# Optimization experiments

Measured on AMD Instinct MI355X. Metric: run time of the kernel, lower is better.

## Reference

```python
import jax, jax.numpy as jnp
import numpy as np
from jax import lax

B, C_IN, C_OUT, KK, KS = 8, 32, 64, 4, 3
D, H, W = 32, 64, 64
PAD = 1

def setup_inputs() -> dict:
    key = jax.random.key(0)
    ks = jax.random.split(key, 12)
    s = 0.02
    return {
        "x": jax.random.normal(ks[0], (B, C_IN, D, H, W), jnp.float32),
        # K candidate conv kernels and biases
        "weight": jax.random.normal(ks[1], (KK, C_OUT, C_IN, KS, KS, KS), jnp.float32) * s,
        "cbias": jnp.zeros((KK, C_OUT), jnp.float32),
        "temperature": jnp.float32(34.0),
        # attention key path: BN(affine, eval-mode) -> GELU -> 1x1 conv (linear)
        "bn1_g": jnp.ones((C_IN,), jnp.float32),
        "bn1_b": jnp.zeros((C_IN,), jnp.float32),
        "w1": jax.random.normal(ks[2], (C_IN, C_IN), jnp.float32) * s,
        "b1": jnp.zeros((C_IN,), jnp.float32),
        "bn2_g": jnp.ones((C_IN,), jnp.float32),
        "bn2_b": jnp.zeros((C_IN,), jnp.float32),
        "w2": jax.random.normal(ks[3], (C_IN, C_IN), jnp.float32) * s,
        "b2": jnp.zeros((C_IN,), jnp.float32),
        "bn3_g": jnp.ones((C_IN,), jnp.float32),
        "bn3_b": jnp.zeros((C_IN,), jnp.float32),
        "w3": jax.random.normal(ks[4], (KK, C_IN), jnp.float32) * s,
        "b3": jnp.zeros((KK,), jnp.float32),
    }

def _attention(p, temperature, bn1_g, bn1_b, w1, b1, bn2_g, bn2_b, w2, b2, bn3_g, bn3_b, w3, b3):
    # p: [B, C] pooled features. 1x1x1 convs on 1x1x1 maps == linear layers.
    gelu = lambda t: jax.nn.gelu(t, approximate=False)  # torch nn.GELU default is erf
    a = gelu(p * bn1_g + bn1_b)          # BN (eval: rm=0, rv=1) + GELU
    a = a @ w1.T + b1
    a = gelu(a * bn2_g + bn2_b)
    a = a @ w2.T + b2
    a = a + p                            # ResidualLayer (plain add)
    a = a * bn3_g + bn3_b
    logits = a @ w3.T + b3               # [B, K]
    return jax.nn.softmax(logits / temperature, axis=1)

def reference(x, weight, cbias, temperature, bn1_g, bn1_b, w1, b1,
              bn2_g, bn2_b, w2, b2, bn3_g, bn3_b, w3, b3):
    # x: [B, C_in, D, H, W]
    p = x.mean(axis=(2, 3, 4))  # AdaptiveAvgPool3d(1)
    attn = _attention(p, temperature, bn1_g, bn1_b, w1, b1,
                      bn2_g, bn2_b, w2, b2, bn3_g, bn3_b, w3, b3)  # [B, K]
    # per-sample aggregated kernels / bias
    agg_w = jnp.einsum('bk,koidhw->boidhw', attn, weight)  # [B, O, I, k, k, k]
    agg_b = attn @ cbias                                    # [B, O]
    # grouped-conv trick (groups=B) == per-sample conv3d -> vmap over batch
    def conv1(xi, wi):
        return lax.conv_general_dilated(
            xi[None], wi, window_strides=(1, 1, 1),
            padding=[(PAD, PAD)] * 3,
            dimension_numbers=('NCDHW', 'OIDHW', 'NCDHW'))[0]
    out = jax.vmap(conv1)(x, agg_w)  # [B, O, D, H, W]
    return out + agg_b[:, :, None, None, None]
```

## Files before the change

kernel.cpp:

```cpp
#include <hip/hip_runtime.h>
#include <hip/hip_bf16.h>
#include <math.h>

#define B_   8
#define CIN  32
#define COUT 64
#define KK_  4
#define DD   32
#define HH   64
#define WW   64
#define HW   (HH*WW)
#define DHW  (DD*HH*WW)

typedef __attribute__((ext_vector_type(8)))  short bf16x8;
typedef __attribute__((ext_vector_type(16))) float f32x16;

__device__ __forceinline__ unsigned short f2bf(float f) {
    union { float f; unsigned int u; } v; v.f = f;
    return (unsigned short)((v.u + 0x7FFFu + ((v.u >> 16) & 1u)) >> 16);
}
__device__ __forceinline__ void gll16(const void* g, void* l) {
    __builtin_amdgcn_global_load_lds(
        (const __attribute__((address_space(1))) void*)g,
        (__attribute__((address_space(3))) void*)l, 16, 0, 0);
}

__global__ __launch_bounds__(256) void transpose_kernel(const float* __restrict__ x,
                                                        unsigned short* __restrict__ xt,
                                                        float* __restrict__ pblk) {
    const int t = threadIdx.x;
    const int r = t >> 6, w = t & 63;
    const int hb = blockIdx.x;
    const int h = (hb << 2) + r;
    const int d = blockIdx.y, b = blockIdx.z;

    const float* xb = x + (size_t)b*CIN*DHW + (size_t)d*HW + (size_t)h*WW + w;
    float f[CIN];
    #pragma unroll
    for (int c = 0; c < CIN; ++c) f[c] = xb[(size_t)c * DHW];

    unsigned int packed[CIN/2];
    #pragma unroll
    for (int c2 = 0; c2 < CIN/2; ++c2) {
        unsigned int lo = f2bf(f[2*c2]);
        unsigned int hi = f2bf(f[2*c2+1]);
        packed[c2] = lo | (hi << 16);
    }
    char* row = (char*)xt + (size_t)((b*DD + d)*HH + h) * 4096;
    #pragma unroll
    for (int q = 0; q < 4; ++q) {
        uint4 v = make_uint4(packed[4*q], packed[4*q+1], packed[4*q+2], packed[4*q+3]);
        *(uint4*)(row + q*1024 + (((w << 4)) ^ (q << 4))) = v;
    }

    #pragma unroll
    for (int off = 32; off > 0; off >>= 1) {
        #pragma unroll
        for (int c = 0; c < CIN; ++c) f[c] += __shfl_xor(f[c], off);
    }
    __shared__ float ws4[4][CIN];
    if ((t & 63) < CIN) ws4[r][t & 63] = f[t & 63];
    __syncthreads();
    if (t < CIN)
        pblk[(size_t)((b*DD + d)*16 + hb)*CIN + t] =
            ws4[0][t] + ws4[1][t] + ws4[2][t] + ws4[3][t];
}

__device__ __forceinline__ float gelu_erf(float v) {
    return 0.5f * v * (1.f + erff(v * 0.70710678118654752f));
}

__global__ void attn_kernel(const float* __restrict__ pblk,
                            const float* __restrict__ temperature,
                            const float* __restrict__ bn1_g, const float* __restrict__ bn1_b,
                            const float* __restrict__ w1,    const float* __restrict__ b1,
                            const float* __restrict__ bn2_g, const float* __restrict__ bn2_b,
                            const float* __restrict__ w2,    const float* __restrict__ b2,
                            const float* __restrict__ bn3_g, const float* __restrict__ bn3_b,
                            const float* __restrict__ w3,    const float* __restrict__ b3,
                            const float* __restrict__ cbias,
                            float* __restrict__ attn_out, float* __restrict__ aggb_out) {
    __shared__ float A[B_][CIN], A2[B_][CIN];
    __shared__ float L[B_][KK_], ATT[B_][KK_];
    const int t = threadIdx.x;
    const int b = t >> 5, c = t & 31;

    float pv = 0.f;
    for (int i = 0; i < DD*16; ++i) pv += pblk[(size_t)(b*DD*16 + i)*CIN + c];
    pv *= (1.f / (float)DHW);

    A[b][c] = gelu_erf(pv * bn1_g[c] + bn1_b[c]);
    __syncthreads();

    float s = b1[c];
    for (int j = 0; j < CIN; ++j) s += A[b][j] * w1[c*CIN + j];
    A2[b][c] = gelu_erf(s * bn2_g[c] + bn2_b[c]);
    __syncthreads();

    float s2 = b2[c];
    for (int j = 0; j < CIN; ++j) s2 += A2[b][j] * w2[c*CIN + j];
    s2 += pv;
    s2 = s2 * bn3_g[c] + bn3_b[c];
    __syncthreads();
    A[b][c] = s2;
    __syncthreads();

    if (c < KK_) {
        float lv = b3[c];
        for (int j = 0; j < CIN; ++j) lv += A[b][j] * w3[c*CIN + j];
        L[b][c] = lv;
    }
    __syncthreads();

    const float T = temperature[0];
    if (c < KK_) {
        float m = fmaxf(fmaxf(L[b][0], L[b][1]), fmaxf(L[b][2], L[b][3]));
        float e = expf((L[b][c] - m) / T);
        float den = 0.f;
        for (int j = 0; j < KK_; ++j) den += expf((L[b][j] - m) / T);
        float av = e / den;
        ATT[b][c] = av;
        attn_out[b*KK_ + c] = av;
    }
    __syncthreads();

    for (int o = c; o < COUT; o += CIN) {
        float sb = 0.f;
        for (int k = 0; k < KK_; ++k) sb += ATT[b][k] * cbias[k*COUT + o];
        aggb_out[b*COUT + o] = sb;
    }
}

__global__ void aggw_kernel(const float* __restrict__ weight,
                            const float* __restrict__ attn,
                            unsigned short* __restrict__ wt) {
    const int idx = blockIdx.x * 256 + threadIdx.x;
    const int ci   = idx & 31;
    const int co   = (idx >> 5) & 63;
    int r          = idx >> 11;
    const int kpos = r % 27;
    const int b    = r / 27;
    float s = 0.f;
    #pragma unroll
    for (int k = 0; k < KK_; ++k)
        s += attn[b*KK_ + k] * weight[((k*COUT + co)*CIN + ci)*27 + kpos];
    wt[idx] = f2bf(s);
}

__global__ __launch_bounds__(128, 1) void conv_mfma(const unsigned short* __restrict__ xt,
                                                    const unsigned short* __restrict__ wt,
                                                    const float* __restrict__ aggb,
                                                    float* __restrict__ out) {
    __shared__ char smem[19 * 4096];
    const int t    = threadIdx.x;
    const int lane = t & 63;
    const int wv   = t >> 6;
    const int lw   = lane & 31, lh = lane >> 5;

    const int id = blockIdx.x;
    const int b  = id & 7;
    const int h  = (id >> 3) & 63;
    const int d0 = ((id >> 9) & 7) << 2;

    const char* xb  = (const char*)xt + (size_t)(b*DD)*HH*4096;
    const char* wtb = (const char*)wt + (size_t)b * 27 * 4096;

    *(uint4*)&smem[18*4096 + t*32]      = make_uint4(0u,0u,0u,0u);
    *(uint4*)&smem[18*4096 + t*32 + 16] = make_uint4(0u,0u,0u,0u);

    for (int rid = wv; rid < 18; rid += 2) {
        const int j = rid / 3, ho = rid % 3;
        const int zd = d0 - 1 + j, yh = h - 1 + ho;
        char* dst = smem + (size_t)(rid << 12);
        if ((unsigned)zd < DD && (unsigned)yh < HH) {
            const char* src = xb + (size_t)(zd*HH + yh)*4096 + lane*16;
            #pragma unroll
            for (int q = 0; q < 4; ++q) gll16(src + (q << 10), dst + (q << 10));
        } else {
            #pragma unroll
            for (int q = 0; q < 4; ++q)
                *(uint4*)(dst + (q << 10) + lane*16) = make_uint4(0u,0u,0u,0u);
        }
    }
    __syncthreads();

    f32x16 acc[2][4];
    #pragma unroll
    for (int cb = 0; cb < 2; ++cb)
        #pragma unroll
        for (int r = 0; r < 4; ++r)
            acc[cb][r] = (f32x16){};

    const int a_off = lw*64 + lh*16;
    const int o0 = lh, o1 = 2 + lh;

    #pragma unroll
    for (int kh = 0; kh < 3; ++kh) {
        #pragma unroll
        for (int kw = 0; kw < 3; ++kw) {
            bf16x8 av[3][2][2];
            #pragma unroll
            for (int kd = 0; kd < 3; ++kd) {
                const char* wk = wtb + (size_t)(((kd*3 + kh)*3 + kw) << 12);
                av[kd][0][0] = *(const bf16x8*)(wk + a_off);
                av[kd][0][1] = *(const bf16x8*)(wk + 32 + a_off);
                av[kd][1][0] = *(const bf16x8*)(wk + 2048 + a_off);
                av[kd][1][1] = *(const bf16x8*)(wk + 2048 + 32 + a_off);
            }

            const int wp  = (wv << 5) + lw + kw - 1;
            const bool oob = ((unsigned)wp >= (unsigned)WW);
            const int wpc = oob ? lw : wp;
            const int sw0 = (o0 << 10) + ((wpc << 4) ^ (o0 << 4));
            const int sw1 = (o1 << 10) + ((wpc << 4) ^ (o1 << 4));
            const int zb  = oob ? 18*4096 : -1;

            bf16x8 bc[6][2];
            #pragma unroll
            for (int j = 0; j < 6; ++j) {
                const int rb = (j*3 + kh) << 12;
                const int base = (zb >= 0) ? zb : rb;
                bc[j][0] = *(const bf16x8*)&smem[base + sw0];
                bc[j][1] = *(const bf16x8*)&smem[base + sw1];
            }

            #pragma unroll
            for (int kd = 0; kd < 3; ++kd) {
                #pragma unroll
                for (int r = 0; r < 4; ++r) {
                    const int j = r + kd;
                    acc[0][r] = __builtin_amdgcn_mfma_f32_32x32x16_bf16(av[kd][0][0], bc[j][0], acc[0][r], 0, 0, 0);
                    acc[0][r] = __builtin_amdgcn_mfma_f32_32x32x16_bf16(av[kd][0][1], bc[j][1], acc[0][r], 0, 0, 0);
                    acc[1][r] = __builtin_amdgcn_mfma_f32_32x32x16_bf16(av[kd][1][0], bc[j][0], acc[1][r], 0, 0, 0);
                    acc[1][r] = __builtin_amdgcn_mfma_f32_32x32x16_bf16(av[kd][1][1], bc[j][1], acc[1][r], 0, 0, 0);
                }
            }
        }
    }

    const float* ab = aggb + b*COUT;
    const int sp0 = h*WW + (wv << 5) + lw;
    #pragma unroll
    for (int cb = 0; cb < 2; ++cb) {
        #pragma unroll
        for (int reg = 0; reg < 16; ++reg) {
            const int co = (cb << 5) + (reg & 3) + ((reg >> 2) << 3) + (lh << 2);
            const float bb = ab[co];
            float* oc = out + ((size_t)(b*COUT + co))*DHW + sp0;
            #pragma unroll
            for (int r = 0; r < 4; ++r)
                oc[(size_t)(d0 + r)*HW] = acc[cb][r][reg] + bb;
        }
    }
}

extern "C" void kernel_launch(void* const* d_in, const int* in_sizes, int n_in,
                              void* d_out, int out_size, void* d_ws, size_t ws_size,
                              hipStream_t stream) {
    const float* x           = (const float*)d_in[0];
    const float* weight      = (const float*)d_in[1];
    const float* cbias       = (const float*)d_in[2];
    const float* temperature = (const float*)d_in[3];
    const float* bn1_g       = (const float*)d_in[4];
    const float* bn1_b       = (const float*)d_in[5];
    const float* w1          = (const float*)d_in[6];
    const float* b1          = (const float*)d_in[7];
    const float* bn2_g       = (const float*)d_in[8];
    const float* bn2_b       = (const float*)d_in[9];
    const float* w2          = (const float*)d_in[10];
    const float* b2          = (const float*)d_in[11];
    const float* bn3_g       = (const float*)d_in[12];
    const float* bn3_b       = (const float*)d_in[13];
    const float* w3          = (const float*)d_in[14];
    const float* b3          = (const float*)d_in[15];
    float* out = (float*)d_out;

    char* ws = (char*)d_ws;
    float*          attn = (float*)(ws + 1024);
    float*          aggb = (float*)(ws + 4096);
    float*          pblk = (float*)(ws + 65536);
    unsigned short* wt   = (unsigned short*)(ws + 622592);
    unsigned short* xt   = (unsigned short*)(ws + 1507328);

    transpose_kernel<<<dim3(HH/4, DD, B_), 256, 0, stream>>>(x, xt, pblk);
    attn_kernel<<<1, 256, 0, stream>>>(pblk, temperature,
                                       bn1_g, bn1_b, w1, b1,
                                       bn2_g, bn2_b, w2, b2,
                                       bn3_g, bn3_b, w3, b3,
                                       cbias, attn, aggb);
    aggw_kernel<<<(B_*27*COUT*CIN)/256, 256, 0, stream>>>(weight, attn, wt);
    conv_mfma<<<dim3(64*8*8), 128, 0, stream>>>(xt, wt, aggb, out);
}
```

Before: 213.4 us.

## Split output channels across four waves per block in conv MFMA kernel

Each conv block now runs 256 threads (4 waves) instead of 128, with the two output-channel halves handled by separate waves rather than one wave accumulating both. This halves accumulator registers per wave and doubles the waves sharing each staged LDS input tile, aiming for more latency hiding, and launch bounds now allow two blocks per CU. The bias is folded into the accumulator init, and s_setprio is raised around the MFMA bursts. The trade-off is that each wave re-reads the same LDS B fragments per channel half, so LDS traffic per output rises.

```diff
diff --git a/kernel.cpp b/kernel.cpp
--- a/kernel.cpp
+++ b/kernel.cpp
@@ -147,14 +147,16 @@
     wt[idx] = f2bf(s);
 }
 
-__global__ __launch_bounds__(128, 1) void conv_mfma(const unsigned short* __restrict__ xt,
+__global__ __launch_bounds__(256, 2) void conv_mfma(const unsigned short* __restrict__ xt,
                                                     const unsigned short* __restrict__ wt,
                                                     const float* __restrict__ aggb,
                                                     float* __restrict__ out) {
     __shared__ char smem[19 * 4096];
     const int t    = threadIdx.x;
     const int lane = t & 63;
-    const int wv   = t >> 6;
+    const int wid  = t >> 6;
+    const int cv   = wid >> 1;
+    const int wv   = wid & 1;
     const int lw   = lane & 31, lh = lane >> 5;
 
     const int id = blockIdx.x;
@@ -163,17 +165,15 @@
     const int d0 = ((id >> 9) & 7) << 2;
 
     const char* xb  = (const char*)xt + (size_t)(b*DD)*HH*4096;
-    const char* wtb = (const char*)wt + (size_t)b * 27 * 4096;
-
-    *(uint4*)&smem[18*4096 + t*32]      = make_uint4(0u,0u,0u,0u);
-    *(uint4*)&smem[18*4096 + t*32 + 16] = make_uint4(0u,0u,0u,0u);
-
-    for (int rid = wv; rid < 18; rid += 2) {
-        const int j = rid / 3, ho = rid % 3;
+    const char* wtb = (const char*)wt + (size_t)b * 27 * 4096 + (cv << 11);
+
+    *(uint4*)&smem[18*4096 + t*16] = make_uint4(0u,0u,0u,0u);
+
+    auto stage_row = [&](int j, int ho) {
         const int zd = d0 - 1 + j, yh = h - 1 + ho;
-        char* dst = smem + (size_t)(rid << 12);
+        char* dst = smem + (size_t)((j*3 + ho) << 12);
         if ((unsigned)zd < DD && (unsigned)yh < HH) {
-            const char* src = xb + (size_t)(zd*HH + yh)*4096 + lane*16;
+            const char* src = xb + ((size_t)(zd*HH + yh) << 12) + lane*16;
             #pragma unroll
             for (int q = 0; q < 4; ++q) gll16(src + (q << 10), dst + (q << 10));
         } else {
@@ -181,76 +181,77 @@
             for (int q = 0; q < 4; ++q)
                 *(uint4*)(dst + (q << 10) + lane*16) = make_uint4(0u,0u,0u,0u);
         }
-    }
-    __syncthreads();
-
-    f32x16 acc[2][4];
-    #pragma unroll
-    for (int cb = 0; cb < 2; ++cb)
-        #pragma unroll
-        for (int r = 0; r < 4; ++r)
-            acc[cb][r] = (f32x16){};
+    };
+    for (int rid = wid; rid < 18; rid += 4)
+        stage_row(rid / 3, rid % 3);
+    __syncthreads();
+
+    f32x16 binit;
+    #pragma unroll
+    for (int reg = 0; reg < 16; ++reg)
+        binit[reg] = aggb[b*COUT + (cv << 5) + (reg & 3) + ((reg >> 2) << 3) + (lh << 2)];
+
+    f32x16 acc[4];
+    #pragma unroll
+    for (int r = 0; r < 4; ++r) acc[r] = binit;
 
     const int a_off = lw*64 + lh*16;
     const int o0 = lh, o1 = 2 + lh;
+    const int ZR = 18*4096;
 
     #pragma unroll
     for (int kh = 0; kh < 3; ++kh) {
+        bf16x8 av[9][2];
+        #pragma unroll
+        for (int kd = 0; kd < 3; ++kd)
+            #pragma unroll
+            for (int kw = 0; kw < 3; ++kw) {
+                const char* wk = wtb + (size_t)(((kd*3 + kh)*3 + kw) << 12);
+                av[kd*3 + kw][0] = *(const bf16x8*)(wk + a_off);
+                av[kd*3 + kw][1] = *(const bf16x8*)(wk + 32 + a_off);
+            }
+
         #pragma unroll
         for (int kw = 0; kw < 3; ++kw) {
-            bf16x8 av[3][2][2];
-            #pragma unroll
-            for (int kd = 0; kd < 3; ++kd) {
-                const char* wk = wtb + (size_t)(((kd*3 + kh)*3 + kw) << 12);
-                av[kd][0][0] = *(const bf16x8*)(wk + a_off);
-                av[kd][0][1] = *(const bf16x8*)(wk + 32 + a_off);
-                av[kd][1][0] = *(const bf16x8*)(wk + 2048 + a_off);
-                av[kd][1][1] = *(const bf16x8*)(wk + 2048 + 32 + a_off);
-            }
-
             const int wp  = (wv << 5) + lw + kw - 1;
             const bool oob = ((unsigned)wp >= (unsigned)WW);
             const int wpc = oob ? lw : wp;
             const int sw0 = (o0 << 10) + ((wpc << 4) ^ (o0 << 4));
             const int sw1 = (o1 << 10) + ((wpc << 4) ^ (o1 << 4));
-            const int zb  = oob ? 18*4096 : -1;
 
             bf16x8 bc[6][2];
             #pragma unroll
             for (int j = 0; j < 6; ++j) {
-                const int rb = (j*3 + kh) << 12;
-                const int base = (zb >= 0) ? zb : rb;
+                const int base = oob ? ZR : ((j*3 + kh) << 12);
                 bc[j][0] = *(const bf16x8*)&smem[base + sw0];
                 bc[j][1] = *(const bf16x8*)&smem[base + sw1];
             }
 
-            #pragma unroll
-            for (int kd = 0; kd < 3; ++kd) {
+            __builtin_amdgcn_s_setprio(1);
+            #pragma unroll
+            for (int khalf = 0; khalf < 2; ++khalf) {
                 #pragma unroll
-                for (int r = 0; r < 4; ++r) {
-                    const int j = r + kd;
-                    acc[0][r] = __builtin_amdgcn_mfma_f32_32x32x16_bf16(av[kd][0][0], bc[j][0], acc[0][r], 0, 0, 0);
-                    acc[0][r] = __builtin_amdgcn_mfma_f32_32x32x16_bf16(av[kd][0][1], bc[j][1], acc[0][r], 0, 0, 0);
-                    acc[1][r] = __builtin_amdgcn_mfma_f32_32x32x16_bf16(av[kd][1][0], bc[j][0], acc[1][r], 0, 0, 0);
-                    acc[1][r] = __builtin_amdgcn_mfma_f32_32x32x16_bf16(av[kd][1][1], bc[j][1], acc[1][r], 0, 0, 0);
+                for (int kd = 0; kd < 3; ++kd) {
+                    #pragma unroll
+                    for (int r = 0; r < 4; ++r) {
+                        const int j = r + kd;
+                        acc[r] = __builtin_amdgcn_mfma_f32_32x32x16_bf16(
+                            av[kd*3 + kw][khalf], bc[j][khalf], acc[r], 0, 0, 0);
+                    }
                 }
             }
+            __builtin_amdgcn_s_setprio(0);
         }
     }
 
-    const float* ab = aggb + b*COUT;
     const int sp0 = h*WW + (wv << 5) + lw;
     #pragma unroll
-    for (int cb = 0; cb < 2; ++cb) {
-        #pragma unroll
-        for (int reg = 0; reg < 16; ++reg) {
-            const int co = (cb << 5) + (reg & 3) + ((reg >> 2) << 3) + (lh << 2);
-            const float bb = ab[co];
-            float* oc = out + ((size_t)(b*COUT + co))*DHW + sp0;
-            #pragma unroll
-            for (int r = 0; r < 4; ++r)
-                oc[(size_t)(d0 + r)*HW] = acc[cb][r][reg] + bb;
-        }
+    for (int reg = 0; reg < 16; ++reg) {
+        const int co = (cv << 5) + (reg & 3) + ((reg >> 2) << 3) + (lh << 2);
+        float* oc = out + ((size_t)(b*COUT + co))*DHW + sp0;
+        #pragma unroll
+        for (int r = 0; r < 4; ++r)
+            oc[(size_t)(d0 + r)*HW] = acc[r][reg];
     }
 }
 
@@ -289,5 +290,5 @@
                                        bn3_g, bn3_b, w3, b3,
                                        cbias, attn, aggb);
     aggw_kernel<<<(B_*27*COUT*CIN)/256, 256, 0, stream>>>(weight, attn, wt);
-    conv_mfma<<<dim3(64*8*8), 128, 0, stream>>>(xt, wt, aggb, out);
-}
+    conv_mfma<<<dim3(4096), 256, 0, stream>>>(xt, wt, aggb, out);
+}
```

Result: faster. 190.9 us (-10.5%).
